# Optimization experiments

Measured on AMD Instinct MI355X. Metric: run time of the kernel, lower is better.

The kernel has to match this reference:

```python
import jax, jax.numpy as jnp
import numpy as np

N, E, C_IN, HID, G, L = 100000, 1600000, 64, 32, 128, 3
NEG_SLOPE = 0.01  # F.leaky_relu default


def setup_inputs() -> dict:
    key = jax.random.key(0)
    ks = jax.random.split(key, 10)
    x = jax.random.normal(ks[0], (N, C_IN), dtype=jnp.float32)
    src = jax.random.randint(ks[1], (E,), 0, N, dtype=jnp.int32)
    dst = jax.random.randint(ks[2], (E,), 0, N, dtype=jnp.int32)
    batch = jnp.sort(jax.random.randint(ks[3], (N,), 0, G, dtype=jnp.int32))
    def glorot(k, fan_in, fan_out):
        lim = np.sqrt(6.0 / (fan_in + fan_out)).astype(np.float32)
        return jax.random.uniform(k, (fan_in, fan_out), jnp.float32, -lim, lim)
    W0 = glorot(ks[4], C_IN, HID); b0 = jnp.zeros((HID,), jnp.float32)
    W1 = glorot(ks[5], HID, HID);  b1 = jnp.zeros((HID,), jnp.float32)
    W2 = glorot(ks[6], HID, HID);  b2 = jnp.zeros((HID,), jnp.float32)
    return {"x": x, "W0": W0, "b0": b0, "W1": W1, "b1": b1,
            "W2": W2, "b2": b2, "src": src, "dst": dst, "batch": batch}


def _gcn_conv(x, W, b, src, dst, dinv):
    # PyG GCNConv: h = x W; aggregate with sym-norm (A + I)
    h = x @ W                                   # [N, H]
    coef = (dinv[src] * dinv[dst])[:, None]     # [E, 1]
    msg = h[src] * coef                         # gather + scale
    agg = jax.ops.segment_sum(msg, dst, num_segments=N)
    agg = agg + h * (dinv * dinv)[:, None]      # self-loop term
    return agg + b


def _mean_pool(x, batch, counts):
    s = jax.ops.segment_sum(x, batch, num_segments=G)
    return s / counts[:, None]


def reference(x, W0, b0, W1, b1, W2, b2, src, dst, batch):
    # degree with self loops (edge weight 1), as PyG gcn_norm does
    deg = jax.ops.segment_sum(jnp.ones((E,), x.dtype), dst, num_segments=N) + 1.0
    dinv = jax.lax.rsqrt(deg)
    counts = jnp.maximum(
        jax.ops.segment_sum(jnp.ones((N,), x.dtype), batch, num_segments=G), 1.0)
    params = [(W0, b0), (W1, b1), (W2, b2)]
    feats = []
    h = x
    for W, b in params:
        h = _gcn_conv(h, W, b, src, dst, dinv)
        h = jax.nn.leaky_relu(h, NEG_SLOPE)
        feats.append(_mean_pool(h, batch, counts))
    merge = jnp.mean(jnp.stack(feats, axis=0), axis=0)  # [G, HID]
    return merge
```

## Files before the change

kernel.cpp:

```cpp
#include <hip/hip_runtime.h>
#include <hip/hip_bf16.h>

#define NN 100000
#define NE 1600000
#define CIN 64
#define HIDN 32
#define NG 128
#define SLOPE 0.01f
#define NBLK 98
#define SCAT_BLOCKS 782
#define MM0_BLOCKS 12500
#define AGG_BLOCKS 3125
#define SCAN_RDY 0x40000000u


__global__ __launch_bounds__(256) void k_rank(const int* __restrict__ dst,
                                              int* __restrict__ deg,
                                              unsigned int* __restrict__ rank) {
  int i = blockIdx.x * 256 + threadIdx.x;
  if (i * 8 >= NE) return;
  int4 a = ((const int4*)dst)[2 * i];
  int4 b = ((const int4*)dst)[2 * i + 1];
  unsigned int r0 = atomicAdd(&deg[a.x], 1);
  unsigned int r1 = atomicAdd(&deg[a.y], 1);
  unsigned int r2 = atomicAdd(&deg[a.z], 1);
  unsigned int r3 = atomicAdd(&deg[a.w], 1);
  unsigned int r4 = atomicAdd(&deg[b.x], 1);
  unsigned int r5 = atomicAdd(&deg[b.y], 1);
  unsigned int r6 = atomicAdd(&deg[b.z], 1);
  unsigned int r7 = atomicAdd(&deg[b.w], 1);
  uint2 packed;
  packed.x = r0 | (r1 << 8) | (r2 << 16) | (r3 << 24);
  packed.y = r4 | (r5 << 8) | (r6 << 16) | (r7 << 24);
  ((uint2*)rank)[i] = packed;
}


__global__ __launch_bounds__(256) void k_scan(const int* __restrict__ deg,
                                              int* __restrict__ rowp,
                                              float* __restrict__ dinv,
                                              const int* __restrict__ batch,
                                              float* __restrict__ cinv,
                                              float* __restrict__ out,
                                              unsigned int* __restrict__ flagA,
                                              unsigned int* __restrict__ flagP) {
  __shared__ int s[256];
  __shared__ int sboff;
  __shared__ int sb[NG + 1];
  const int t = threadIdx.x;
  const int b = blockIdx.x;
  const int base = b * 1024 + t * 4;
  int d0 = 0, d1 = 0, d2 = 0, d3 = 0;
  if (base < NN) { d0 = deg[base]; dinv[base] = rsqrtf((float)d0 + 1.0f); }
  if (base + 1 < NN) { d1 = deg[base + 1]; dinv[base + 1] = rsqrtf((float)d1 + 1.0f); }
  if (base + 2 < NN) { d2 = deg[base + 2]; dinv[base + 2] = rsqrtf((float)d2 + 1.0f); }
  if (base + 3 < NN) { d3 = deg[base + 3]; dinv[base + 3] = rsqrtf((float)d3 + 1.0f); }
  const int ts = d0 + d1 + d2 + d3;
  s[t] = ts;
  __syncthreads();
  for (int o = 1; o < 256; o <<= 1) {
    int v = (t >= o) ? s[t - o] : 0;
    __syncthreads();
    s[t] += v;
    __syncthreads();
  }
  const int total = s[255];
  if (t == 0) {
    __threadfence();
    atomicExch(&flagA[b], (unsigned)total | SCAN_RDY);
    unsigned run = 0;
    if (b > 0) {
      int j = b - 1;
      while (j >= 0) {
        unsigned p = atomicAdd(&flagP[j], 0u);
        if (p & SCAN_RDY) { run += p & 0x3FFFFFFFu; break; }
        unsigned a = atomicAdd(&flagA[j], 0u);
        if (a & SCAN_RDY) { run += a & 0x3FFFFFFFu; --j; }
      }
    }
    __threadfence();
    atomicExch(&flagP[b], (run + (unsigned)total) | SCAN_RDY);
    sboff = (int)run;
  }
  __syncthreads();
  int run = sboff + s[t] - ts;
  if (base < NN) { rowp[base] = run; run += d0; }
  if (base + 1 < NN) { rowp[base + 1] = run; run += d1; }
  if (base + 2 < NN) { rowp[base + 2] = run; run += d2; }
  if (base + 3 < NN) { rowp[base + 3] = run; run += d3; }
  if (b == NBLK - 1 && t == 255) rowp[NN] = run;

  if (b == 0) {
    if (t <= NG) {
      int lo = 0, hi = NN;
      while (lo < hi) {
        int mid = (lo + hi) >> 1;
        if (batch[mid] < t) lo = mid + 1; else hi = mid;
      }
      sb[t] = lo;
    }
    for (int i = t; i < NG * HIDN; i += 256) out[i] = 0.f;
    __syncthreads();
    if (t < NG) {
      int c = sb[t + 1] - sb[t];
      cinv[t] = 1.0f / (3.0f * fmaxf((float)c, 1.0f));
    }
  }
}


__global__ __launch_bounds__(256) void k_sm(const int* __restrict__ src,
                                            const int* __restrict__ dst,
                                            const unsigned int* __restrict__ rank,
                                            const int* __restrict__ rowp,
                                            int* __restrict__ col,
                                            const float* __restrict__ x,
                                            const float* __restrict__ W0,
                                            const float* __restrict__ dinv,
                                            __hip_bfloat16* __restrict__ hs) {
  __shared__ float sW[CIN * HIDN];
  if (blockIdx.x < SCAT_BLOCKS) {
    int i = blockIdx.x * 256 + threadIdx.x;
    if (i * 8 >= NE) return;
    int4 da = ((const int4*)dst)[2 * i];
    int4 db = ((const int4*)dst)[2 * i + 1];
    uint2 rr = ((const uint2*)rank)[i];
    int4 sa = ((const int4*)src)[2 * i];
    int4 sb = ((const int4*)src)[2 * i + 1];
    col[rowp[da.x] + (int)(rr.x & 0xff)] = sa.x;
    col[rowp[da.y] + (int)((rr.x >> 8) & 0xff)] = sa.y;
    col[rowp[da.z] + (int)((rr.x >> 16) & 0xff)] = sa.z;
    col[rowp[da.w] + (int)(rr.x >> 24)] = sa.w;
    col[rowp[db.x] + (int)(rr.y & 0xff)] = sb.x;
    col[rowp[db.y] + (int)((rr.y >> 8) & 0xff)] = sb.y;
    col[rowp[db.z] + (int)((rr.y >> 16) & 0xff)] = sb.z;
    col[rowp[db.w] + (int)(rr.y >> 24)] = sb.w;
    return;
  }
  int t = threadIdx.x;
  for (int i = t; i < CIN * HIDN; i += 256) sW[i] = W0[i];
  __syncthreads();
  int gid = (blockIdx.x - SCAT_BLOCKS) * 256 + t;
  int node = gid >> 5;
  int f = gid & 31;
  const float* xr = x + node * CIN;
  float acc = 0.f;
#pragma unroll
  for (int k = 0; k < CIN; ++k) acc += xr[k] * sW[k * HIDN + f];
  hs[node * HIDN + f] = __float2bfloat16(acc * dinv[node]);
}


template <int FUSE>
__global__ __launch_bounds__(256) void k_agg(const __hip_bfloat16* __restrict__ hs,
                                             const int* __restrict__ rowp,
                                             const int* __restrict__ col,
                                             const float* __restrict__ dinv,
                                             const int* __restrict__ batch,
                                             const float* __restrict__ cinv,
                                             const float* __restrict__ bias,
                                             const float* __restrict__ Wn,
                                             __hip_bfloat16* __restrict__ hs_next,
                                             float* __restrict__ pool) {
  __shared__ float vrow[32][32];
  __shared__ float sWn[FUSE ? HIDN * HIDN : 1];
  const int t = threadIdx.x;
  const int f = t & 31;
  const int sub = t >> 5;
  const int base = blockIdx.x * 32;

  if (FUSE) {
#pragma unroll
    for (int i = 0; i < 4; ++i) sWn[t + i * 256] = Wn[t + i * 256];
  }

  const float bf = bias[f];
  float pacc = 0.f;
  int gcur = -1;
#pragma unroll
  for (int it = 0; it < 4; ++it) {
    const int i = base + it * 8 + sub;
    float acc = __bfloat162float(hs[i * HIDN + f]);
    const int rs = rowp[i];
    const int re = rowp[i + 1];
    int e = rs;
    const int nfull = (re - rs) >> 3;
    if (nfull > 0) {
      int c0 = __builtin_nontemporal_load(col + e);
      int c1 = __builtin_nontemporal_load(col + e + 1);
      int c2 = __builtin_nontemporal_load(col + e + 2);
      int c3 = __builtin_nontemporal_load(col + e + 3);
      int c4 = __builtin_nontemporal_load(col + e + 4);
      int c5 = __builtin_nontemporal_load(col + e + 5);
      int c6 = __builtin_nontemporal_load(col + e + 6);
      int c7 = __builtin_nontemporal_load(col + e + 7);
      for (int bi = 1; bi < nfull; ++bi) {
        const int n0 = __builtin_nontemporal_load(col + e + 8);
        const int n1 = __builtin_nontemporal_load(col + e + 9);
        const int n2 = __builtin_nontemporal_load(col + e + 10);
        const int n3 = __builtin_nontemporal_load(col + e + 11);
        const int n4 = __builtin_nontemporal_load(col + e + 12);
        const int n5 = __builtin_nontemporal_load(col + e + 13);
        const int n6 = __builtin_nontemporal_load(col + e + 14);
        const int n7 = __builtin_nontemporal_load(col + e + 15);
        const float v0 = __bfloat162float(hs[c0 * HIDN + f]);
        const float v1 = __bfloat162float(hs[c1 * HIDN + f]);
        const float v2 = __bfloat162float(hs[c2 * HIDN + f]);
        const float v3 = __bfloat162float(hs[c3 * HIDN + f]);
        const float v4 = __bfloat162float(hs[c4 * HIDN + f]);
        const float v5 = __bfloat162float(hs[c5 * HIDN + f]);
        const float v6 = __bfloat162float(hs[c6 * HIDN + f]);
        const float v7 = __bfloat162float(hs[c7 * HIDN + f]);
        acc += ((v0 + v1) + (v2 + v3)) + ((v4 + v5) + (v6 + v7));
        c0 = n0; c1 = n1; c2 = n2; c3 = n3; c4 = n4; c5 = n5; c6 = n6; c7 = n7;
        e += 8;
      }
      const float v0 = __bfloat162float(hs[c0 * HIDN + f]);
      const float v1 = __bfloat162float(hs[c1 * HIDN + f]);
      const float v2 = __bfloat162float(hs[c2 * HIDN + f]);
      const float v3 = __bfloat162float(hs[c3 * HIDN + f]);
      const float v4 = __bfloat162float(hs[c4 * HIDN + f]);
      const float v5 = __bfloat162float(hs[c5 * HIDN + f]);
      const float v6 = __bfloat162float(hs[c6 * HIDN + f]);
      const float v7 = __bfloat162float(hs[c7 * HIDN + f]);
      acc += ((v0 + v1) + (v2 + v3)) + ((v4 + v5) + (v6 + v7));
      e += 8;
    }
    if (re - e >= 4) {
      const int c0 = __builtin_nontemporal_load(col + e);
      const int c1 = __builtin_nontemporal_load(col + e + 1);
      const int c2 = __builtin_nontemporal_load(col + e + 2);
      const int c3 = __builtin_nontemporal_load(col + e + 3);
      const float v0 = __bfloat162float(hs[c0 * HIDN + f]);
      const float v1 = __bfloat162float(hs[c1 * HIDN + f]);
      const float v2 = __bfloat162float(hs[c2 * HIDN + f]);
      const float v3 = __bfloat162float(hs[c3 * HIDN + f]);
      acc += (v0 + v1) + (v2 + v3);
      e += 4;
    }
    for (; e < re; ++e) acc += __bfloat162float(hs[col[e] * HIDN + f]);
    float v = acc * dinv[i] + bf;
    v = v > 0.f ? v : SLOPE * v;
    if (FUSE) vrow[it * 8 + sub][f] = v;
    const int g = batch[i];
    if (g != gcur) {
      if (gcur >= 0) unsafeAtomicAdd(&pool[gcur * HIDN + f], pacc * cinv[gcur]);
      gcur = g;
      pacc = 0.f;
    }
    pacc += v;
  }
  if (gcur >= 0) unsafeAtomicAdd(&pool[gcur * HIDN + f], pacc * cinv[gcur]);

  if (FUSE) {
    __syncthreads();
#pragma unroll
    for (int q = 0; q < 4; ++q) {
      const int li = sub * 4 + q;
      const int i = base + li;
      float a = 0.f;
#pragma unroll
      for (int k = 0; k < HIDN; ++k) a += vrow[li][k] * sWn[k * HIDN + f];
      hs_next[i * HIDN + f] = __float2bfloat16(a * dinv[i]);
    }
  }
}


extern "C" void kernel_launch(void* const* d_in, const int* in_sizes, int n_in,
                              void* d_out, int out_size, void* d_ws, size_t ws_size,
                              hipStream_t stream) {
  const float* x = (const float*)d_in[0];
  const float* W0 = (const float*)d_in[1];
  const float* b0 = (const float*)d_in[2];
  const float* W1 = (const float*)d_in[3];
  const float* b1 = (const float*)d_in[4];
  const float* W2 = (const float*)d_in[5];
  const float* b2 = (const float*)d_in[6];
  const int* src = (const int*)d_in[7];
  const int* dst = (const int*)d_in[8];
  const int* batch = (const int*)d_in[9];
  float* out = (float*)d_out;

  char* ws = (char*)d_ws;
  auto carve = [&](size_t bytes) -> char* {
    char* p = ws;
    ws += (bytes + 255) & ~(size_t)255;
    return p;
  };
  unsigned int* flagA = (unsigned int*)carve(512);
  unsigned int* flagP = (unsigned int*)carve(512);
  int* deg = (int*)carve(NN * 4);
  unsigned int* rank = (unsigned int*)carve((size_t)NE);
  int* rowp = (int*)carve((NN + 1) * 4);
  float* dinv = (float*)carve(NN * 4);
  float* cinv = (float*)carve(NG * 4);
  int* col = (int*)carve((size_t)NE * 4);
  __hip_bfloat16* hsA = (__hip_bfloat16*)carve((size_t)NN * HIDN * 2);
  __hip_bfloat16* hsB = (__hip_bfloat16*)carve((size_t)NN * HIDN * 2);

  hipMemsetAsync(flagA, 0, 1024 + ((NN * 4 + 255) & ~255), stream);

  k_rank<<<SCAT_BLOCKS, 256, 0, stream>>>(dst, deg, rank);
  k_scan<<<NBLK, 256, 0, stream>>>(deg, rowp, dinv, batch, cinv, out, flagA, flagP);
  k_sm<<<SCAT_BLOCKS + MM0_BLOCKS, 256, 0, stream>>>(src, dst, rank, rowp, col,
                                                     x, W0, dinv, hsA);
  k_agg<1><<<AGG_BLOCKS, 256, 0, stream>>>(hsA, rowp, col, dinv, batch, cinv,
                                           b0, W1, hsB, out);
  k_agg<1><<<AGG_BLOCKS, 256, 0, stream>>>(hsB, rowp, col, dinv, batch, cinv,
                                           b1, W2, hsA, out);
  k_agg<0><<<AGG_BLOCKS, 256, 0, stream>>>(hsA, rowp, col, dinv, batch, cinv,
                                           b2, nullptr, nullptr, out);
}
```

Baseline: 414.2 us.

## Fuse all stages into one persistent cooperative kernel with grid syncs

Replaces the six separate kernel launches and the memset with a single cooperative persistent kernel that uses grid-wide syncs between the degree count, scan, CSR scatter, first matmul and the three aggregation layers. The decoupled look-back scan is replaced by a per-block scan plus a grid sync and a serial sum over block totals. This is meant to remove launch gaps and per-kernel ramp costs. In exchange, the grid is capped by occupancy (2048 blocks at most), so work runs in grid-stride loops with grid-barrier overhead and possibly lower parallelism in the gather phases.

Measured after the change: 1.545 ms. +273.1%, slower.

```diff
diff --git a/kernel.cpp b/kernel.cpp
--- a/kernel.cpp
+++ b/kernel.cpp
@@ -1,208 +1,83 @@
 #include <hip/hip_runtime.h>
 #include <hip/hip_bf16.h>
+#include <hip/hip_cooperative_groups.h>
+
+namespace cg = cooperative_groups;
 
 #define NN 100000
 #define NE 1600000
+#define NQ (NE / 8)
 #define CIN 64
 #define HIDN 32
 #define NG 128
 #define SLOPE 0.01f
 #define NBLK 98
-#define SCAT_BLOCKS 782
-#define MM0_BLOCKS 12500
-#define AGG_BLOCKS 3125
-#define SCAN_RDY 0x40000000u
-
-
-__global__ __launch_bounds__(256) void k_rank(const int* __restrict__ dst,
-                                              int* __restrict__ deg,
-                                              unsigned int* __restrict__ rank) {
-  int i = blockIdx.x * 256 + threadIdx.x;
-  if (i * 8 >= NE) return;
-  int4 a = ((const int4*)dst)[2 * i];
-  int4 b = ((const int4*)dst)[2 * i + 1];
-  unsigned int r0 = atomicAdd(&deg[a.x], 1);
-  unsigned int r1 = atomicAdd(&deg[a.y], 1);
-  unsigned int r2 = atomicAdd(&deg[a.z], 1);
-  unsigned int r3 = atomicAdd(&deg[a.w], 1);
-  unsigned int r4 = atomicAdd(&deg[b.x], 1);
-  unsigned int r5 = atomicAdd(&deg[b.y], 1);
-  unsigned int r6 = atomicAdd(&deg[b.z], 1);
-  unsigned int r7 = atomicAdd(&deg[b.w], 1);
-  uint2 packed;
-  packed.x = r0 | (r1 << 8) | (r2 << 16) | (r3 << 24);
-  packed.y = r4 | (r5 << 8) | (r6 << 16) | (r7 << 24);
-  ((uint2*)rank)[i] = packed;
-}
-
-
-__global__ __launch_bounds__(256) void k_scan(const int* __restrict__ deg,
-                                              int* __restrict__ rowp,
-                                              float* __restrict__ dinv,
-                                              const int* __restrict__ batch,
-                                              float* __restrict__ cinv,
-                                              float* __restrict__ out,
-                                              unsigned int* __restrict__ flagA,
-                                              unsigned int* __restrict__ flagP) {
-  __shared__ int s[256];
-  __shared__ int sboff;
-  __shared__ int sb[NG + 1];
-  const int t = threadIdx.x;
-  const int b = blockIdx.x;
-  const int base = b * 1024 + t * 4;
-  int d0 = 0, d1 = 0, d2 = 0, d3 = 0;
-  if (base < NN) { d0 = deg[base]; dinv[base] = rsqrtf((float)d0 + 1.0f); }
-  if (base + 1 < NN) { d1 = deg[base + 1]; dinv[base + 1] = rsqrtf((float)d1 + 1.0f); }
-  if (base + 2 < NN) { d2 = deg[base + 2]; dinv[base + 2] = rsqrtf((float)d2 + 1.0f); }
-  if (base + 3 < NN) { d3 = deg[base + 3]; dinv[base + 3] = rsqrtf((float)d3 + 1.0f); }
-  const int ts = d0 + d1 + d2 + d3;
-  s[t] = ts;
-  __syncthreads();
-  for (int o = 1; o < 256; o <<= 1) {
-    int v = (t >= o) ? s[t - o] : 0;
-    __syncthreads();
-    s[t] += v;
-    __syncthreads();
-  }
-  const int total = s[255];
-  if (t == 0) {
-    __threadfence();
-    atomicExch(&flagA[b], (unsigned)total | SCAN_RDY);
-    unsigned run = 0;
-    if (b > 0) {
-      int j = b - 1;
-      while (j >= 0) {
-        unsigned p = atomicAdd(&flagP[j], 0u);
-        if (p & SCAN_RDY) { run += p & 0x3FFFFFFFu; break; }
-        unsigned a = atomicAdd(&flagA[j], 0u);
-        if (a & SCAN_RDY) { run += a & 0x3FFFFFFFu; --j; }
-      }
-    }
-    __threadfence();
-    atomicExch(&flagP[b], (run + (unsigned)total) | SCAN_RDY);
-    sboff = (int)run;
-  }
-  __syncthreads();
-  int run = sboff + s[t] - ts;
-  if (base < NN) { rowp[base] = run; run += d0; }
-  if (base + 1 < NN) { rowp[base + 1] = run; run += d1; }
-  if (base + 2 < NN) { rowp[base + 2] = run; run += d2; }
-  if (base + 3 < NN) { rowp[base + 3] = run; run += d3; }
-  if (b == NBLK - 1 && t == 255) rowp[NN] = run;
-
-  if (b == 0) {
-    if (t <= NG) {
-      int lo = 0, hi = NN;
-      while (lo < hi) {
-        int mid = (lo + hi) >> 1;
-        if (batch[mid] < t) lo = mid + 1; else hi = mid;
-      }
-      sb[t] = lo;
-    }
-    for (int i = t; i < NG * HIDN; i += 256) out[i] = 0.f;
-    __syncthreads();
-    if (t < NG) {
-      int c = sb[t + 1] - sb[t];
-      cinv[t] = 1.0f / (3.0f * fmaxf((float)c, 1.0f));
-    }
-  }
-}
-
-
-__global__ __launch_bounds__(256) void k_sm(const int* __restrict__ src,
-                                            const int* __restrict__ dst,
-                                            const unsigned int* __restrict__ rank,
-                                            const int* __restrict__ rowp,
-                                            int* __restrict__ col,
-                                            const float* __restrict__ x,
-                                            const float* __restrict__ W0,
-                                            const float* __restrict__ dinv,
-                                            __hip_bfloat16* __restrict__ hs) {
-  __shared__ float sW[CIN * HIDN];
-  if (blockIdx.x < SCAT_BLOCKS) {
-    int i = blockIdx.x * 256 + threadIdx.x;
-    if (i * 8 >= NE) return;
-    int4 da = ((const int4*)dst)[2 * i];
-    int4 db = ((const int4*)dst)[2 * i + 1];
-    uint2 rr = ((const uint2*)rank)[i];
-    int4 sa = ((const int4*)src)[2 * i];
-    int4 sb = ((const int4*)src)[2 * i + 1];
-    col[rowp[da.x] + (int)(rr.x & 0xff)] = sa.x;
-    col[rowp[da.y] + (int)((rr.x >> 8) & 0xff)] = sa.y;
-    col[rowp[da.z] + (int)((rr.x >> 16) & 0xff)] = sa.z;
-    col[rowp[da.w] + (int)(rr.x >> 24)] = sa.w;
-    col[rowp[db.x] + (int)(rr.y & 0xff)] = sb.x;
-    col[rowp[db.y] + (int)((rr.y >> 8) & 0xff)] = sb.y;
-    col[rowp[db.z] + (int)((rr.y >> 16) & 0xff)] = sb.z;
-    col[rowp[db.w] + (int)(rr.y >> 24)] = sb.w;
-    return;
-  }
-  int t = threadIdx.x;
-  for (int i = t; i < CIN * HIDN; i += 256) sW[i] = W0[i];
-  __syncthreads();
-  int gid = (blockIdx.x - SCAT_BLOCKS) * 256 + t;
-  int node = gid >> 5;
-  int f = gid & 31;
-  const float* xr = x + node * CIN;
-  float acc = 0.f;
-#pragma unroll
-  for (int k = 0; k < CIN; ++k) acc += xr[k] * sW[k * HIDN + f];
-  hs[node * HIDN + f] = __float2bfloat16(acc * dinv[node]);
-}
+#define MM_UNITS 12500
+#define AGG_UNITS 3125
 
 
 template <int FUSE>
-__global__ __launch_bounds__(256) void k_agg(const __hip_bfloat16* __restrict__ hs,
-                                             const int* __restrict__ rowp,
-                                             const int* __restrict__ col,
-                                             const float* __restrict__ dinv,
-                                             const int* __restrict__ batch,
-                                             const float* __restrict__ cinv,
-                                             const float* __restrict__ bias,
-                                             const float* __restrict__ Wn,
-                                             __hip_bfloat16* __restrict__ hs_next,
-                                             float* __restrict__ pool) {
-  __shared__ float vrow[32][32];
-  __shared__ float sWn[FUSE ? HIDN * HIDN : 1];
-  const int t = threadIdx.x;
+__device__ void agg_phase(int b, int t, int gsize,
+                          const __hip_bfloat16* __restrict__ hs,
+                          const int* __restrict__ rowp,
+                          const int* __restrict__ col,
+                          const float* __restrict__ dinv,
+                          const int* __restrict__ batch,
+                          const float* __restrict__ cinv,
+                          const float* __restrict__ bias,
+                          const float* __restrict__ Wn,
+                          __hip_bfloat16* __restrict__ hs_next,
+                          float* __restrict__ pool,
+                          float (*vrow)[32], float* sWn) {
   const int f = t & 31;
   const int sub = t >> 5;
-  const int base = blockIdx.x * 32;
-
   if (FUSE) {
+    for (int i = t; i < HIDN * HIDN; i += 256) sWn[i] = Wn[i];
+  }
+  const float bf = bias[f];
+  for (int u = b; u < AGG_UNITS; u += gsize) {
+    __syncthreads();
+    const int base = u * 32;
+    float pacc = 0.f;
+    int gcur = -1;
 #pragma unroll
-    for (int i = 0; i < 4; ++i) sWn[t + i * 256] = Wn[t + i * 256];
-  }
-
-  const float bf = bias[f];
-  float pacc = 0.f;
-  int gcur = -1;
-#pragma unroll
-  for (int it = 0; it < 4; ++it) {
-    const int i = base + it * 8 + sub;
-    float acc = __bfloat162float(hs[i * HIDN + f]);
-    const int rs = rowp[i];
-    const int re = rowp[i + 1];
-    int e = rs;
-    const int nfull = (re - rs) >> 3;
-    if (nfull > 0) {
-      int c0 = __builtin_nontemporal_load(col + e);
-      int c1 = __builtin_nontemporal_load(col + e + 1);
-      int c2 = __builtin_nontemporal_load(col + e + 2);
-      int c3 = __builtin_nontemporal_load(col + e + 3);
-      int c4 = __builtin_nontemporal_load(col + e + 4);
-      int c5 = __builtin_nontemporal_load(col + e + 5);
-      int c6 = __builtin_nontemporal_load(col + e + 6);
-      int c7 = __builtin_nontemporal_load(col + e + 7);
-      for (int bi = 1; bi < nfull; ++bi) {
-        const int n0 = __builtin_nontemporal_load(col + e + 8);
-        const int n1 = __builtin_nontemporal_load(col + e + 9);
-        const int n2 = __builtin_nontemporal_load(col + e + 10);
-        const int n3 = __builtin_nontemporal_load(col + e + 11);
-        const int n4 = __builtin_nontemporal_load(col + e + 12);
-        const int n5 = __builtin_nontemporal_load(col + e + 13);
-        const int n6 = __builtin_nontemporal_load(col + e + 14);
-        const int n7 = __builtin_nontemporal_load(col + e + 15);
+    for (int it = 0; it < 4; ++it) {
+      const int i = base + it * 8 + sub;
+      float acc = __bfloat162float(hs[i * HIDN + f]);
+      const int rs = rowp[i];
+      const int re = rowp[i + 1];
+      int e = rs;
+      const int nfull = (re - rs) >> 3;
+      if (nfull > 0) {
+        int c0 = __builtin_nontemporal_load(col + e);
+        int c1 = __builtin_nontemporal_load(col + e + 1);
+        int c2 = __builtin_nontemporal_load(col + e + 2);
+        int c3 = __builtin_nontemporal_load(col + e + 3);
+        int c4 = __builtin_nontemporal_load(col + e + 4);
+        int c5 = __builtin_nontemporal_load(col + e + 5);
+        int c6 = __builtin_nontemporal_load(col + e + 6);
+        int c7 = __builtin_nontemporal_load(col + e + 7);
+        for (int bi = 1; bi < nfull; ++bi) {
+          const int n0 = __builtin_nontemporal_load(col + e + 8);
+          const int n1 = __builtin_nontemporal_load(col + e + 9);
+          const int n2 = __builtin_nontemporal_load(col + e + 10);
+          const int n3 = __builtin_nontemporal_load(col + e + 11);
+          const int n4 = __builtin_nontemporal_load(col + e + 12);
+          const int n5 = __builtin_nontemporal_load(col + e + 13);
+          const int n6 = __builtin_nontemporal_load(col + e + 14);
+          const int n7 = __builtin_nontemporal_load(col + e + 15);
+          const float v0 = __bfloat162float(hs[c0 * HIDN + f]);
+          const float v1 = __bfloat162float(hs[c1 * HIDN + f]);
+          const float v2 = __bfloat162float(hs[c2 * HIDN + f]);
+          const float v3 = __bfloat162float(hs[c3 * HIDN + f]);
+          const float v4 = __bfloat162float(hs[c4 * HIDN + f]);
+          const float v5 = __bfloat162float(hs[c5 * HIDN + f]);
+          const float v6 = __bfloat162float(hs[c6 * HIDN + f]);
+          const float v7 = __bfloat162float(hs[c7 * HIDN + f]);
+          acc += ((v0 + v1) + (v2 + v3)) + ((v4 + v5) + (v6 + v7));
+          c0 = n0; c1 = n1; c2 = n2; c3 = n3; c4 = n4; c5 = n5; c6 = n6; c7 = n7;
+          e += 8;
+        }
         const float v0 = __bfloat162float(hs[c0 * HIDN + f]);
         const float v1 = __bfloat162float(hs[c1 * HIDN + f]);
         const float v2 = __bfloat162float(hs[c2 * HIDN + f]);
@@ -212,58 +87,182 @@
         const float v6 = __bfloat162float(hs[c6 * HIDN + f]);
         const float v7 = __bfloat162float(hs[c7 * HIDN + f]);
         acc += ((v0 + v1) + (v2 + v3)) + ((v4 + v5) + (v6 + v7));
-        c0 = n0; c1 = n1; c2 = n2; c3 = n3; c4 = n4; c5 = n5; c6 = n6; c7 = n7;
         e += 8;
       }
-      const float v0 = __bfloat162float(hs[c0 * HIDN + f]);
-      const float v1 = __bfloat162float(hs[c1 * HIDN + f]);
-      const float v2 = __bfloat162float(hs[c2 * HIDN + f]);
-      const float v3 = __bfloat162float(hs[c3 * HIDN + f]);
-      const float v4 = __bfloat162float(hs[c4 * HIDN + f]);
-      const float v5 = __bfloat162float(hs[c5 * HIDN + f]);
-      const float v6 = __bfloat162float(hs[c6 * HIDN + f]);
-      const float v7 = __bfloat162float(hs[c7 * HIDN + f]);
-      acc += ((v0 + v1) + (v2 + v3)) + ((v4 + v5) + (v6 + v7));
-      e += 8;
-    }
-    if (re - e >= 4) {
-      const int c0 = __builtin_nontemporal_load(col + e);
-      const int c1 = __builtin_nontemporal_load(col + e + 1);
-      const int c2 = __builtin_nontemporal_load(col + e + 2);
-      const int c3 = __builtin_nontemporal_load(col + e + 3);
-      const float v0 = __bfloat162float(hs[c0 * HIDN + f]);
-      const float v1 = __bfloat162float(hs[c1 * HIDN + f]);
-      const float v2 = __bfloat162float(hs[c2 * HIDN + f]);
-      const float v3 = __bfloat162float(hs[c3 * HIDN + f]);
-      acc += (v0 + v1) + (v2 + v3);
-      e += 4;
-    }
-    for (; e < re; ++e) acc += __bfloat162float(hs[col[e] * HIDN + f]);
-    float v = acc * dinv[i] + bf;
-    v = v > 0.f ? v : SLOPE * v;
-    if (FUSE) vrow[it * 8 + sub][f] = v;
-    const int g = batch[i];
-    if (g != gcur) {
-      if (gcur >= 0) unsafeAtomicAdd(&pool[gcur * HIDN + f], pacc * cinv[gcur]);
-      gcur = g;
-      pacc = 0.f;
-    }
-    pacc += v;
-  }
-  if (gcur >= 0) unsafeAtomicAdd(&pool[gcur * HIDN + f], pacc * cinv[gcur]);
-
-  if (FUSE) {
+      if (re - e >= 4) {
+        const int c0 = __builtin_nontemporal_load(col + e);
+        const int c1 = __builtin_nontemporal_load(col + e + 1);
+        const int c2 = __builtin_nontemporal_load(col + e + 2);
+        const int c3 = __builtin_nontemporal_load(col + e + 3);
+        const float v0 = __bfloat162float(hs[c0 * HIDN + f]);
+        const float v1 = __bfloat162float(hs[c1 * HIDN + f]);
+        const float v2 = __bfloat162float(hs[c2 * HIDN + f]);
+        const float v3 = __bfloat162float(hs[c3 * HIDN + f]);
+        acc += (v0 + v1) + (v2 + v3);
+        e += 4;
+      }
+      for (; e < re; ++e) acc += __bfloat162float(hs[col[e] * HIDN + f]);
+      float v = acc * dinv[i] + bf;
+      v = v > 0.f ? v : SLOPE * v;
+      if (FUSE) vrow[it * 8 + sub][f] = v;
+      const int g = batch[i];
+      if (g != gcur) {
+        if (gcur >= 0) unsafeAtomicAdd(&pool[gcur * HIDN + f], pacc * cinv[gcur]);
+        gcur = g;
+        pacc = 0.f;
+      }
+      pacc += v;
+    }
+    if (gcur >= 0) unsafeAtomicAdd(&pool[gcur * HIDN + f], pacc * cinv[gcur]);
+
+    if (FUSE) {
+      __syncthreads();
+#pragma unroll
+      for (int q = 0; q < 4; ++q) {
+        const int li = sub * 4 + q;
+        const int i = base + li;
+        float a = 0.f;
+#pragma unroll
+        for (int k = 0; k < HIDN; ++k) a += vrow[li][k] * sWn[k * HIDN + f];
+        hs_next[i * HIDN + f] = __float2bfloat16(a * dinv[i]);
+      }
+    }
+  }
+}
+
+
+__global__ __launch_bounds__(256, 8) void k_all(
+    const int* __restrict__ src, const int* __restrict__ dst,
+    const int* __restrict__ batch, const float* __restrict__ x,
+    const float* __restrict__ W0, const float* __restrict__ b0,
+    const float* __restrict__ W1, const float* __restrict__ b1,
+    const float* __restrict__ W2, const float* __restrict__ b2,
+    float* __restrict__ out,
+    int* __restrict__ deg, unsigned int* __restrict__ rank,
+    int* __restrict__ rowp, int* __restrict__ bsum,
+    float* __restrict__ dinv, float* __restrict__ cinv,
+    int* __restrict__ col,
+    __hip_bfloat16* __restrict__ hsA, __hip_bfloat16* __restrict__ hsB) {
+  cg::grid_group gg = cg::this_grid();
+  __shared__ float sWbuf[CIN * HIDN];
+  __shared__ float vrow[32][32];
+  __shared__ float sWn[HIDN * HIDN];
+  int* sscan = (int*)sWbuf;
+  int* sb = (int*)sWbuf + 256;
+
+  const int t = threadIdx.x;
+  const int b = blockIdx.x;
+  const int gsize = gridDim.x;
+  const int gtid = b * 256 + t;
+  const int gthreads = gsize * 256;
+
+  for (int i = gtid; i < NN; i += gthreads) deg[i] = 0;
+  for (int i = gtid; i < NG * HIDN; i += gthreads) out[i] = 0.f;
+  gg.sync();
+
+  for (int u = gtid; u < NQ; u += gthreads) {
+    int4 a = ((const int4*)dst)[2 * u];
+    int4 bb = ((const int4*)dst)[2 * u + 1];
+    unsigned r0 = atomicAdd(&deg[a.x], 1);
+    unsigned r1 = atomicAdd(&deg[a.y], 1);
+    unsigned r2 = atomicAdd(&deg[a.z], 1);
+    unsigned r3 = atomicAdd(&deg[a.w], 1);
+    unsigned r4 = atomicAdd(&deg[bb.x], 1);
+    unsigned r5 = atomicAdd(&deg[bb.y], 1);
+    unsigned r6 = atomicAdd(&deg[bb.z], 1);
+    unsigned r7 = atomicAdd(&deg[bb.w], 1);
+    uint2 packed;
+    packed.x = r0 | (r1 << 8) | (r2 << 16) | (r3 << 24);
+    packed.y = r4 | (r5 << 8) | (r6 << 16) | (r7 << 24);
+    ((uint2*)rank)[u] = packed;
+  }
+  gg.sync();
+
+  int d0 = 0, d1 = 0, d2 = 0, d3 = 0, ts = 0, incl = 0;
+  if (b < NBLK) {
+    const int base = b * 1024 + t * 4;
+    if (base < NN) { d0 = deg[base]; dinv[base] = rsqrtf((float)d0 + 1.0f); }
+    if (base + 1 < NN) { d1 = deg[base + 1]; dinv[base + 1] = rsqrtf((float)d1 + 1.0f); }
+    if (base + 2 < NN) { d2 = deg[base + 2]; dinv[base + 2] = rsqrtf((float)d2 + 1.0f); }
+    if (base + 3 < NN) { d3 = deg[base + 3]; dinv[base + 3] = rsqrtf((float)d3 + 1.0f); }
+    ts = d0 + d1 + d2 + d3;
+    sscan[t] = ts;
     __syncthreads();
+    for (int o = 1; o < 256; o <<= 1) {
+      int v = (t >= o) ? sscan[t - o] : 0;
+      __syncthreads();
+      sscan[t] += v;
+      __syncthreads();
+    }
+    incl = sscan[t];
+    if (t == 255) bsum[b] = incl;
+  } else if (b == NBLK) {
+    if (t <= NG) {
+      int lo = 0, hi = NN;
+      while (lo < hi) {
+        int mid = (lo + hi) >> 1;
+        if (batch[mid] < t) lo = mid + 1; else hi = mid;
+      }
+      sb[t] = lo;
+    }
+    __syncthreads();
+    if (t < NG) {
+      int c = sb[t + 1] - sb[t];
+      cinv[t] = 1.0f / (3.0f * fmaxf((float)c, 1.0f));
+    }
+  }
+  gg.sync();
+
+  if (b < NBLK) {
+    if (t < NBLK) sscan[t] = bsum[t];
+    __syncthreads();
+    int off = 0;
+    for (int j = 0; j < b; ++j) off += sscan[j];
+    int run = off + incl - ts;
+    const int base = b * 1024 + t * 4;
+    if (base < NN) { rowp[base] = run; run += d0; }
+    if (base + 1 < NN) { rowp[base + 1] = run; run += d1; }
+    if (base + 2 < NN) { rowp[base + 2] = run; run += d2; }
+    if (base + 3 < NN) { rowp[base + 3] = run; run += d3; }
+    if (b == NBLK - 1 && t == 255) rowp[NN] = run;
+  }
+  gg.sync();
+
+  for (int u = gtid; u < NQ; u += gthreads) {
+    int4 da = ((const int4*)dst)[2 * u];
+    int4 db = ((const int4*)dst)[2 * u + 1];
+    uint2 rr = ((const uint2*)rank)[u];
+    int4 sa = ((const int4*)src)[2 * u];
+    int4 sbb = ((const int4*)src)[2 * u + 1];
+    col[rowp[da.x] + (int)(rr.x & 0xff)] = sa.x;
+    col[rowp[da.y] + (int)((rr.x >> 8) & 0xff)] = sa.y;
+    col[rowp[da.z] + (int)((rr.x >> 16) & 0xff)] = sa.z;
+    col[rowp[da.w] + (int)(rr.x >> 24)] = sa.w;
+    col[rowp[db.x] + (int)(rr.y & 0xff)] = sbb.x;
+    col[rowp[db.y] + (int)((rr.y >> 8) & 0xff)] = sbb.y;
+    col[rowp[db.z] + (int)((rr.y >> 16) & 0xff)] = sbb.z;
+    col[rowp[db.w] + (int)(rr.y >> 24)] = sbb.w;
+  }
+  __syncthreads();
+  for (int i = t; i < CIN * HIDN; i += 256) sWbuf[i] = W0[i];
+  __syncthreads();
+  for (int g = b; g < MM_UNITS; g += gsize) {
+    const int gid2 = g * 256 + t;
+    const int node = gid2 >> 5;
+    const int f = gid2 & 31;
+    const float* xr = x + node * CIN;
+    float acc = 0.f;
 #pragma unroll
-    for (int q = 0; q < 4; ++q) {
-      const int li = sub * 4 + q;
-      const int i = base + li;
-      float a = 0.f;
-#pragma unroll
-      for (int k = 0; k < HIDN; ++k) a += vrow[li][k] * sWn[k * HIDN + f];
-      hs_next[i * HIDN + f] = __float2bfloat16(a * dinv[i]);
-    }
-  }
+    for (int k = 0; k < CIN; ++k) acc += xr[k] * sWbuf[k * HIDN + f];
+    hsA[node * HIDN + f] = __float2bfloat16(acc * dinv[node]);
+  }
+  gg.sync();
+
+  agg_phase<1>(b, t, gsize, hsA, rowp, col, dinv, batch, cinv, b0, W1, hsB, out, vrow, sWn);
+  gg.sync();
+  agg_phase<1>(b, t, gsize, hsB, rowp, col, dinv, batch, cinv, b1, W2, hsA, out, vrow, sWn);
+  gg.sync();
+  agg_phase<0>(b, t, gsize, hsA, rowp, col, dinv, batch, cinv, b2, nullptr, nullptr, out, vrow, sWn);
 }
 
 
@@ -288,27 +287,27 @@
     ws += (bytes + 255) & ~(size_t)255;
     return p;
   };
-  unsigned int* flagA = (unsigned int*)carve(512);
-  unsigned int* flagP = (unsigned int*)carve(512);
   int* deg = (int*)carve(NN * 4);
   unsigned int* rank = (unsigned int*)carve((size_t)NE);
   int* rowp = (int*)carve((NN + 1) * 4);
+  int* bsum = (int*)carve(128 * 4);
   float* dinv = (float*)carve(NN * 4);
   float* cinv = (float*)carve(NG * 4);
   int* col = (int*)carve((size_t)NE * 4);
   __hip_bfloat16* hsA = (__hip_bfloat16*)carve((size_t)NN * HIDN * 2);
   __hip_bfloat16* hsB = (__hip_bfloat16*)carve((size_t)NN * HIDN * 2);
 
-  hipMemsetAsync(flagA, 0, 1024 + ((NN * 4 + 255) & ~255), stream);
-
-  k_rank<<<SCAT_BLOCKS, 256, 0, stream>>>(dst, deg, rank);
-  k_scan<<<NBLK, 256, 0, stream>>>(deg, rowp, dinv, batch, cinv, out, flagA, flagP);
-  k_sm<<<SCAT_BLOCKS + MM0_BLOCKS, 256, 0, stream>>>(src, dst, rank, rowp, col,
-                                                     x, W0, dinv, hsA);
-  k_agg<1><<<AGG_BLOCKS, 256, 0, stream>>>(hsA, rowp, col, dinv, batch, cinv,
-                                           b0, W1, hsB, out);
-  k_agg<1><<<AGG_BLOCKS, 256, 0, stream>>>(hsB, rowp, col, dinv, batch, cinv,
-                                           b1, W2, hsA, out);
-  k_agg<0><<<AGG_BLOCKS, 256, 0, stream>>>(hsA, rowp, col, dinv, batch, cinv,
-                                           b2, nullptr, nullptr, out);
+  int bpc = 0;
+  if (hipOccupancyMaxActiveBlocksPerMultiprocessor(&bpc, k_all, 256, 0) != hipSuccess || bpc < 1)
+    bpc = 1;
+  int grid = bpc * 256;
+  if (grid > 2048) grid = 2048;
+  if (grid < 256) grid = 256;
+
+  void* kargs[] = {
+      (void*)&src, (void*)&dst, (void*)&batch, (void*)&x,
+      (void*)&W0, (void*)&b0, (void*)&W1, (void*)&b1, (void*)&W2, (void*)&b2,
+      (void*)&out, (void*)&deg, (void*)&rank, (void*)&rowp, (void*)&bsum,
+      (void*)&dinv, (void*)&cinv, (void*)&col, (void*)&hsA, (void*)&hsB};
+  hipLaunchCooperativeKernel(k_all, dim3(grid), dim3(256), kargs, 0, stream);
 }
```
